# Optimization experiments

Measured on AMD Instinct MI355X. Metric: run time of the kernel, lower is better.

## Reference

```python
import jax, jax.numpy as jnp
import numpy as np

VOC, MEM, NSLOTS, NSENT, MAXLEN, QLEN, ANSLEN, B = 32000, 128, 20, 128, 32, 16, 8, 64


def _xavier(k, shape):
    fan_out, fan_in = shape
    std = jnp.sqrt(2.0 / (fan_in + fan_out))
    return (jax.random.normal(k, shape, jnp.float32) * std).astype(jnp.float32)


def setup_inputs() -> dict:
    key = jax.random.key(0)
    ks = jax.random.split(key, 12)
    inp = {}
    inp["input_ids"] = jax.random.randint(ks[0], (B, NSENT, MAXLEN), 0, VOC)
    inp["question"] = jax.random.randint(ks[1], (B, QLEN), 0, VOC)
    inp["ans"] = jax.random.randint(ks[2], (B, ANSLEN, 2), 0, VOC)
    E = jax.random.normal(ks[3], (VOC, MEM), jnp.float32)
    inp["E"] = E.at[0].set(0.0)  # padding_idx=0
    inp["Uw"] = _xavier(ks[4], (MEM, MEM)); inp["Ub"] = jnp.zeros((MEM,), jnp.float32)
    inp["Vw"] = _xavier(ks[5], (MEM, MEM)); inp["Vb"] = jnp.zeros((MEM,), jnp.float32)
    inp["Ww"] = _xavier(ks[6], (MEM, MEM)); inp["Wb"] = jnp.zeros((MEM,), jnp.float32)
    inp["slot_keys"] = jax.random.normal(ks[7], (NSLOTS, MEM), jnp.float32)  # self.w
    inp["Hw"] = _xavier(ks[8], (MEM, MEM)); inp["Hb"] = jnp.zeros((MEM,), jnp.float32)
    return inp


def reference(input_ids, question, ans, E, Uw, Ub, Vw, Vb, Ww, Wb, slot_keys, Hw, Hb):
    E0 = E.at[0].set(0.0)  # padding row stays zero
    bsz = input_ids.shape[0]
    n_sent = input_ids.shape[1]
    tok = input_ids.reshape(bsz, -1)
    # original indexes s[:, t, :] for t < n_sent over the flattened story
    s = E0[tok[:, :n_sent]]                       # [B, T, m]
    Ws = jnp.einsum('btm,nm->btn', s, Ww) + Wb    # precompute W(s_t): [B, T, m]
    Vkey = slot_keys @ Vw.T + Vb                  # [J, m]

    def step(mem, xs):
        # mem: [B, J, m]
        s_t, ws_t = xs                            # [B, m], [B, m]
        g = jax.nn.sigmoid(jnp.einsum('bm,bjm->bj', s_t, mem) + s_t @ slot_keys.T)  # [B, J]
        h_cand = jax.nn.relu(
            jnp.einsum('bjm,nm->bjn', mem, Uw) + Ub
            + Vkey[None, :, :] + ws_t[:, None, :]
        )  # dropout is identity in eval mode
        mem = mem + g[..., None] * h_cand
        # torch.norm(mem_j): global Frobenius norm over (batch, mem) per slot
        norms = jnp.sqrt(jnp.sum(mem * mem, axis=(0, 2), keepdims=True))
        return mem / norms, None

    mem0 = jnp.zeros((bsz, slot_keys.shape[0], s.shape[-1]), s.dtype)
    h, _ = jax.lax.scan(step, mem0, (jnp.swapaxes(s, 0, 1), jnp.swapaxes(Ws, 0, 1)))
    # output module
    q = E0[question].mean(1)                      # [B, m]
    a1 = E0[ans[:, :, 0]].mean(1)                 # [B, m]
    a2 = E0[ans[:, :, 1]].mean(1)                 # [B, m]
    p = jax.nn.softmax(jnp.einsum('bjm,bm->bj', h, q), axis=-1)   # [B, J]
    u = jnp.einsum('bj,bjm->bm', p, h)            # [B, m]
    r = jax.nn.relu(q + u @ Hw.T + Hb)            # [B, m]
    y1 = jnp.sum(r * a1, axis=1)
    y2 = jnp.sum(r * a2, axis=1)
    return jax.nn.softmax(jnp.stack((y1, y2), axis=1), axis=1)
```

## Files before the change

### kernel.cpp

```cpp
#include <hip/hip_runtime.h>
#include <math.h>


typedef __attribute__((ext_vector_type(8)))  short bf16x8;
typedef __attribute__((ext_vector_type(16))) float f32x16;
typedef __attribute__((ext_vector_type(2)))  float f32x2;

__device__ __forceinline__ unsigned short f2bh(float x) {
    unsigned int u = __float_as_uint(x);
    u += 0x7FFFu + ((u >> 16) & 1u);
    return (unsigned short)(u >> 16);
}
__device__ __forceinline__ unsigned int packtr(float lo, float hi) {
    return (__float_as_uint(lo) >> 16) | (__float_as_uint(hi) & 0xFFFF0000u);
}
__device__ __forceinline__ float blo(unsigned int w) { return __uint_as_float(w << 16); }
__device__ __forceinline__ float bhi(unsigned int w) { return __uint_as_float(w & 0xFFFF0000u); }

__device__ __forceinline__ f32x2 pkfma(f32x2 a, f32x2 b, f32x2 c) {
    return __builtin_elementwise_fma(a, b, c);
}
__device__ __forceinline__ f32x2 pkmax0(f32x2 a) {
    return __builtin_elementwise_max(a, (f32x2){0.f, 0.f});
}

#if __has_builtin(__builtin_amdgcn_fdot2_f32_bf16)
typedef __attribute__((ext_vector_type(2))) __bf16 bf16x2v;
__device__ __forceinline__ float dot2bf(unsigned int a, unsigned int b, float c) {
    return __builtin_amdgcn_fdot2_f32_bf16(
        __builtin_bit_cast(bf16x2v, a), __builtin_bit_cast(bf16x2v, b), c, false);
}
#else
__device__ __forceinline__ float dot2bf(unsigned int a, unsigned int b, float c) {
    return fmaf(bhi(a), bhi(b), fmaf(blo(a), blo(b), c));
}
#endif

template<int CTRL>
__device__ __forceinline__ float dpp_add0(float x) {
    int y = __builtin_amdgcn_update_dpp(0, __float_as_int(x), CTRL, 0xF, 0xF, true);
    return x + __int_as_float(y);
}
__device__ __forceinline__ float dpp_xor1_move(float x) {
    int y = __builtin_amdgcn_update_dpp(0, __float_as_int(x), 0xB1, 0xF, 0xF, true);
    return __int_as_float(y);
}

#define LDS_BARRIER() do {                                   \
    asm volatile("s_waitcnt lgkmcnt(0)" ::: "memory");       \
    __builtin_amdgcn_s_barrier();                            \
    asm volatile("" ::: "memory");                           \
} while (0)

__global__ __launch_bounds__(128) void prep_kernel(
    const int* __restrict__ ids, const int* __restrict__ ques, const int* __restrict__ ans,
    const float* __restrict__ E, const float* __restrict__ Ww, const float* __restrict__ Wb,
    const float* __restrict__ Vw, const float* __restrict__ Vb, const float* __restrict__ skeys,
    unsigned short* __restrict__ sT2, float* __restrict__ WsT, float* __restrict__ vkey,
    float* __restrict__ qv, float* __restrict__ a1v, float* __restrict__ a2v,
    float* __restrict__ SK)
{
    const int bi  = blockIdx.x;
    const int tid = threadIdx.x;
    __shared__ float s_l[8][132];
    __shared__ float sk_l[20 * 132];
    __shared__ float k_l[128];
    if (bi < 1024) {
        const int b = bi >> 4;
        const int g = bi & 15;
        for (int r = tid; r < 2560; r += 128) sk_l[(r >> 7) * 132 + (r & 127)] = skeys[r];
        for (int tt = 0; tt < 8; ++tt) {
            const int t     = g * 8 + tt;
            const int token = ids[b * 4096 + t];
            const float v   = E[token * 128 + tid];
            s_l[tt][tid] = v;
            sT2[(t * 64 + b) * 128 + tid] = f2bh(v);
        }
        __syncthreads();
        float acc[8];
        const float wbn = Wb[tid];
        #pragma unroll
        for (int i = 0; i < 8; ++i) acc[i] = wbn;
        const float4* wrow = (const float4*)(Ww + tid * 128);
        for (int m4 = 0; m4 < 32; ++m4) {
            const float4 w = wrow[m4];
            #pragma unroll
            for (int tt = 0; tt < 8; ++tt) {
                acc[tt] += s_l[tt][m4*4+0]*w.x + s_l[tt][m4*4+1]*w.y
                         + s_l[tt][m4*4+2]*w.z + s_l[tt][m4*4+3]*w.w;
            }
        }
        for (int tt = 0; tt < 8; ++tt)
            WsT[((g*8+tt) * 64 + b) * 128 + tid] = acc[tt];
        for (int idx = tid; idx < 160; idx += 128) {
            const int tt = idx / 20;
            const int jj = idx - tt * 20;
            float d = 0.f;
            for (int m = 0; m < 128; ++m) d += s_l[tt][m] * sk_l[jj * 132 + m];
            SK[(jj * 128 + (g*8 + tt)) * 64 + b] = d;
        }
    } else if (bi < 1044) {
        const int j = bi - 1024;
        k_l[tid] = skeys[j * 128 + tid];
        __syncthreads();
        float acc = Vb[tid];
        const float4* vrow = (const float4*)(Vw + tid * 128);
        for (int m4 = 0; m4 < 32; ++m4) {
            const float4 w = vrow[m4];
            acc += k_l[m4*4]*w.x + k_l[m4*4+1]*w.y + k_l[m4*4+2]*w.z + k_l[m4*4+3]*w.w;
        }
        vkey[j * 128 + tid] = acc;
    } else {
        const int b = bi - 1044;
        float sq = 0.f, s1 = 0.f, s2 = 0.f;
        for (int i = 0; i < 16; ++i) sq += E[ques[b*16+i] * 128 + tid];
        for (int i = 0; i < 8;  ++i) s1 += E[ans[(b*8+i)*2+0] * 128 + tid];
        for (int i = 0; i < 8;  ++i) s2 += E[ans[(b*8+i)*2+1] * 128 + tid];
        qv [b*128+tid] = sq * (1.f/16.f);
        a1v[b*128+tid] = s1 * 0.125f;
        a2v[b*128+tid] = s2 * 0.125f;
    }
}

__global__ __launch_bounds__(512, 1) void scan_kernel(
    const unsigned short* __restrict__ sT2, const float* __restrict__ WsT,
    const float* __restrict__ vkey, const float* __restrict__ Uw,
    const float* __restrict__ Ub, const float* __restrict__ SK,
    float* __restrict__ h_out)
{
    __shared__ unsigned short AB[64 * 136];
    __shared__ float g_l[64];
    __shared__ float wred[8];

    const int j    = blockIdx.x;
    const int tid  = threadIdx.x;
    const int wave = tid >> 6;
    const int lane = tid & 63;
    const int l32  = lane & 31;
    const int q    = lane >> 5;
    const int bt2  = wave & 1;
    const int nt2  = wave >> 1;
    const int n    = nt2 * 32 + l32;
    const int gb   = tid >> 3;
    const int gm   = (tid & 7) * 16;
    const bool evenl = ((l32 & 1) == 0);

    bf16x8 b_h[8];
    {
        const int k0 = q * 8;
        #pragma unroll
        for (int kc = 0; kc < 8; ++kc) {
            const float4* src = (const float4*)(Uw + n * 128 + kc * 16 + k0);
            const float4 v0 = src[0], v1 = src[1];
            const float xs[8] = {v0.x,v0.y,v0.z,v0.w, v1.x,v1.y,v1.z,v1.w};
            #pragma unroll
            for (int e = 0; e < 8; ++e) b_h[kc][e] = (short)f2bh(xs[e]);
        }
    }
    for (int i = tid; i < 64 * 136 / 2; i += 512) ((unsigned int*)AB)[i] = 0u;
    const float ubv = Ub[n] + vkey[j * 128 + n];

    unsigned woffB[16];
    #pragma unroll
    for (int r = 0; r < 16; ++r) {
        const int brow = bt2*32 + 4*q + (r & 3) + 8*(r >> 2);
        woffB[r] = (unsigned)((brow * 128 + n) * 4);
    }
    const unsigned soffB = (unsigned)((gb * 128 + gm) * 2);
    const unsigned koffB = (unsigned)(gb * 4);
    const char* SKj = (const char*)SK + (size_t)j * 32768;
    unsigned* const wdst = (unsigned*)((char*)AB
        + (bt2*32 + 4*q + ((l32 & 1) << 4)) * 272 + ((n & ~1) * 2));

    f32x2 xprev2[8];
    #pragma unroll
    for (int p = 0; p < 8; ++p) xprev2[p] = (f32x2){0.f, 0.f};
#define XV(k) ((k) & 1 ? xprev2[(k) >> 1].y : xprev2[(k) >> 1].x)

    uint4 svA0, svA1, svB0, svB1;
    float skvA, skvB;
    float wsv[16];
    {
        const char* pS = (const char*)sT2 + soffB;
        svA0 = *(const uint4*)(pS); svA1 = *(const uint4*)(pS + 16);
        skvA = *(const float*)(SKj + koffB);
        const char* pW = (const char*)WsT;
        #pragma unroll
        for (int r = 0; r < 16; ++r) wsv[r] = *(const float*)(pW + woffB[r]);
    }
    __syncthreads();

    float inv_s = 1.f;

#define SCAN_STEP(T_CUR, Sc0,Sc1,SKc, Sn0,Sn1,SKn)                             \
    {                                                                          \
        const int tn = (T_CUR < 127) ? (T_CUR) + 1 : 127;                      \
                        \
        {                                                                      \
            const char* pS = (const char*)sT2 + (size_t)tn * 16384 + soffB;    \
            Sn0 = *(const uint4*)(pS); Sn1 = *(const uint4*)(pS + 16);         \
            SKn = *(const float*)(SKj + (size_t)tn * 256 + koffB);             \
        }                                                                      \
               \
        {                                                                      \
            const uint4* u4 = (const uint4*)(AB + gb * 136 + gm);              \
            const uint4 w0 = u4[0], w1 = u4[1];                                \
            float d0 = dot2bf(w0.x, Sc0.x, 0.f);                               \
            float d1 = dot2bf(w0.y, Sc0.y, 0.f);                               \
            float d2 = dot2bf(w0.z, Sc0.z, 0.f);                               \
            float d3 = dot2bf(w0.w, Sc0.w, 0.f);                               \
            d0 = dot2bf(w1.x, Sc1.x, d0);                                      \
            d1 = dot2bf(w1.y, Sc1.y, d1);                                      \
            d2 = dot2bf(w1.z, Sc1.z, d2);                                      \
            d3 = dot2bf(w1.w, Sc1.w, d3);                                      \
            float dg = (d0 + d1) + (d2 + d3);                                  \
            dg = dpp_add0<0x111>(dg);                           \
            dg = dpp_add0<0x112>(dg);                           \
            dg = dpp_add0<0x114>(dg);          \
            if ((tid & 7) == 7) {                                              \
                const float e = __expf(-(inv_s * dg + SKc));                   \
                g_l[gb] = __builtin_amdgcn_rcpf(1.f + e);                      \
            }                                                                  \
        }                                                                      \
                         \
        f32x16 acc0 = {0.f,0.f,0.f,0.f,0.f,0.f,0.f,0.f,                        \
                       0.f,0.f,0.f,0.f,0.f,0.f,0.f,0.f};                       \
        f32x16 acc1 = acc0;                                                    \
        {                                                                      \
            const unsigned short* arow = AB + (bt2*32 + l32) * 136 + q * 8;    \
            _Pragma("unroll")                                                  \
            for (int kc = 0; kc < 8; ++kc) {                                   \
                const bf16x8 a = *(const bf16x8*)(arow + kc * 16);             \
                if (kc & 1) acc1 = __builtin_amdgcn_mfma_f32_32x32x16_bf16(a, b_h[kc], acc1, 0, 0, 0); \
                else        acc0 = __builtin_amdgcn_mfma_f32_32x32x16_bf16(a, b_h[kc], acc0, 0, 0, 0); \
            }                                                                  \
            acc0 += acc1;    \
        }                                                                      \
        LDS_BARRIER();                 \
                 \
        const float4 gA = *(const float4*)(g_l + bt2*32 + 4*q + 0);            \
        const float4 gB = *(const float4*)(g_l + bt2*32 + 4*q + 8);            \
        const float4 gC = *(const float4*)(g_l + bt2*32 + 4*q + 16);           \
        const float4 gD = *(const float4*)(g_l + bt2*32 + 4*q + 24);           \
        const f32x2 g2[8] = {{gA.x,gA.y},{gA.z,gA.w},{gB.x,gB.y},{gB.z,gB.w},  \
                             {gC.x,gC.y},{gC.z,gC.w},{gD.x,gD.y},{gD.z,gD.w}}; \
        const f32x2 inv2 = {inv_s, inv_s};                                     \
        const f32x2 ub2  = {ubv, ubv};                                         \
        f32x2 ssqv = {0.f, 0.f};                                               \
        _Pragma("unroll")                                                      \
        for (int p = 0; p < 8; ++p) {                                          \
            const f32x2 am = {acc0[2*p], acc0[2*p+1]};                         \
            const f32x2 wu = (f32x2){wsv[2*p], wsv[2*p+1]} + ub2;              \
            f32x2 hr = pkfma(inv2, am, wu);                                    \
            hr = pkmax0(hr);                                       \
            const f32x2 x = pkfma(inv2, xprev2[p], hr * g2[p]);                \
            xprev2[p] = x;                                \
            ssqv = pkfma(x, x, ssqv);                                          \
        }                                                                      \
               \
        _Pragma("unroll")                                                      \
        for (int i = 0; i < 8; ++i) {                                          \
            const float xa = XV(i);                                            \
            const float xb = XV(i + 8);                                        \
            const float sa = dpp_xor1_move(xa);                                \
            const float sb = dpp_xor1_move(xb);                                \
            const float lo = evenl ? xa : sb;                                  \
            const float hi = evenl ? sa : xb;                                  \
            wdst[((i & 3) + 8 * (i >> 2)) * 68] = packtr(lo, hi);              \
        }                                                                      \
            \
        {                                                                      \
            const char* pW = (const char*)WsT + (size_t)tn * 32768;            \
            _Pragma("unroll")                                                  \
            for (int r = 0; r < 16; ++r)                                       \
                wsv[r] = *(const float*)(pW + woffB[r]);                       \
        }                                                                      \
                 \
        float ssq = ssqv.x + ssqv.y;                                           \
        ssq = dpp_add0<0x111>(ssq);                             \
        ssq = dpp_add0<0x112>(ssq);                             \
        ssq = dpp_add0<0x114>(ssq);                             \
        ssq = dpp_add0<0x118>(ssq);       \
        ssq = dpp_add0<0x142>(ssq);     \
        ssq = dpp_add0<0x143>(ssq);          \
        if (lane == 63) wred[wave] = ssq;                                      \
        LDS_BARRIER();     \
        const float4 w0 = *(const float4*)(wred);                              \
        const float4 w1 = *(const float4*)(wred + 4);                          \
        const float4 ws4 = w0 + w1;                                            \
        inv_s = __builtin_amdgcn_rsqf((ws4.x + ws4.y) + (ws4.z + ws4.w));      \
    }

    for (int t = 0; t < 128; t += 2) {
        SCAN_STEP(t,     svA0,svA1,skvA, svB0,svB1,skvB)
        SCAN_STEP(t + 1, svB0,svB1,skvB, svA0,svA1,skvA)
    }
#undef SCAN_STEP

    #pragma unroll
    for (int r = 0; r < 16; ++r) {
        const int brow = bt2*32 + 4*q + (r & 3) + 8*(r >> 2);
        h_out[(brow*20 + j)*128 + n] = inv_s * XV(r);
    }
#undef XV
}

__global__ __launch_bounds__(128) void final_kernel(
    const float* __restrict__ h, const float* __restrict__ qv,
    const float* __restrict__ a1v, const float* __restrict__ a2v,
    const float* __restrict__ Hw, const float* __restrict__ Hb,
    float* __restrict__ out)
{
    const int b   = blockIdx.x;
    const int tid = threadIdx.x;
    __shared__ float hb[20][128];
    __shared__ float ql[128];
    __shared__ float ul[128];
    __shared__ float pl[20];
    __shared__ float lgt[20];
    __shared__ float red1[2], red2[2];

    for (int jj = 0; jj < 20; ++jj) hb[jj][tid] = h[(b*20+jj)*128 + tid];
    ql[tid] = qv[b*128 + tid];
    __syncthreads();
    if (tid < 20) {
        float d = 0.f;
        for (int m = 0; m < 128; ++m) d += hb[tid][m] * ql[m];
        lgt[tid] = d;
    }
    __syncthreads();
    if (tid == 0) {
        float mx = lgt[0];
        for (int jj = 1; jj < 20; ++jj) mx = fmaxf(mx, lgt[jj]);
        float s = 0.f;
        for (int jj = 0; jj < 20; ++jj) { const float e = expf(lgt[jj]-mx); pl[jj] = e; s += e; }
        const float is = 1.f / s;
        for (int jj = 0; jj < 20; ++jj) pl[jj] *= is;
    }
    __syncthreads();
    float u = 0.f;
    for (int jj = 0; jj < 20; ++jj) u += pl[jj] * hb[jj][tid];
    ul[tid] = u;
    __syncthreads();
    float acc = ql[tid] + Hb[tid];
    const float4* hwr = (const float4*)(Hw + tid*128);
    for (int m4 = 0; m4 < 32; ++m4) {
        const float4 w = hwr[m4];
        acc += ul[m4*4]*w.x + ul[m4*4+1]*w.y + ul[m4*4+2]*w.z + ul[m4*4+3]*w.w;
    }
    const float r  = fmaxf(acc, 0.f);
    float y1 = r * a1v[b*128+tid];
    float y2 = r * a2v[b*128+tid];
    #pragma unroll
    for (int mask = 1; mask < 64; mask <<= 1) {
        y1 += __shfl_xor(y1, mask, 64);
        y2 += __shfl_xor(y2, mask, 64);
    }
    if ((tid & 63) == 0) { red1[tid>>6] = y1; red2[tid>>6] = y2; }
    __syncthreads();
    if (tid == 0) {
        const float z1 = red1[0] + red1[1];
        const float z2 = red2[0] + red2[1];
        const float mx = fmaxf(z1, z2);
        const float e1 = expf(z1-mx), e2 = expf(z2-mx);
        const float s  = e1 + e2;
        out[b*2+0] = e1 / s;
        out[b*2+1] = e2 / s;
    }
}

extern "C" void kernel_launch(void* const* d_in, const int* in_sizes, int n_in,
                              void* d_out, int out_size, void* d_ws, size_t ws_size,
                              hipStream_t stream)
{
    const int*   ids  = (const int*)  d_in[0];
    const int*   ques = (const int*)  d_in[1];
    const int*   ans  = (const int*)  d_in[2];
    const float* E    = (const float*)d_in[3];
    const float* Uw   = (const float*)d_in[4];
    const float* Ubv  = (const float*)d_in[5];
    const float* Vw   = (const float*)d_in[6];
    const float* Vb   = (const float*)d_in[7];
    const float* Ww   = (const float*)d_in[8];
    const float* Wb   = (const float*)d_in[9];
    const float* sk   = (const float*)d_in[10];
    const float* Hw   = (const float*)d_in[11];
    const float* Hb   = (const float*)d_in[12];

    float* ws   = (float*)d_ws;
    unsigned short* sT2 = (unsigned short*)ws;
    float* WsT  = ws    + 524288;
    float* vkey = WsT   + 1048576;
    float* qv   = vkey  + 2560;
    float* a1v  = qv    + 8192;
    float* a2v  = a1v   + 8192;
    float* h    = a2v   + 8192;
    float* SK   = h     + 163840;

    prep_kernel<<<1108, 128, 0, stream>>>(ids, ques, ans, E, Ww, Wb, Vw, Vb, sk,
                                          sT2, WsT, vkey, qv, a1v, a2v, SK);
    scan_kernel<<<20, 512, 0, stream>>>(sT2, WsT, vkey, Uw, Ubv, SK, h);
    final_kernel<<<64, 128, 0, stream>>>(h, qv, a1v, a2v, Hw, Hb, (float*)d_out);
}
```

Before: 261.2 us.

## Halve scan block to 256 threads, each wave computing two N-tiles

The sequential scan kernel now uses 4 waves instead of 8. Each wave computes two 32-column output tiles with two MFMA chains, and the gate dot product is split across 4 lanes instead of 8. The goal is cheaper per-step barriers and cross-wave reductions on the 128-step serial chain, and more independent MFMA work per wave. The cost is twice the per-wave MFMA and elementwise work on the critical path, plus higher register pressure.

```diff
diff --git a/kernel.cpp b/kernel.cpp
--- a/kernel.cpp
+++ b/kernel.cpp
@@ -122,7 +122,7 @@
     }
 }
 
-__global__ __launch_bounds__(512, 1) void scan_kernel(
+__global__ __launch_bounds__(256, 1) void scan_kernel(
     const unsigned short* __restrict__ sT2, const float* __restrict__ WsT,
     const float* __restrict__ vkey, const float* __restrict__ Uw,
     const float* __restrict__ Ub, const float* __restrict__ SK,
@@ -130,7 +130,7 @@
 {
     __shared__ unsigned short AB[64 * 136];
     __shared__ float g_l[64];
-    __shared__ float wred[8];
+    __shared__ float wred[4];
 
     const int j    = blockIdx.x;
     const int tid  = threadIdx.x;
@@ -139,102 +139,131 @@
     const int l32  = lane & 31;
     const int q    = lane >> 5;
     const int bt2  = wave & 1;
-    const int nt2  = wave >> 1;
-    const int n    = nt2 * 32 + l32;
-    const int gb   = tid >> 3;
-    const int gm   = (tid & 7) * 16;
+    const int nt1  = wave >> 1;
+    const int nA   = nt1 * 64 + l32;
+    const int gb   = tid >> 2;
+    const int gm32 = (tid & 3) * 32;
     const bool evenl = ((l32 & 1) == 0);
 
-    bf16x8 b_h[8];
+    bf16x8 b_hA[8], b_hB[8];
     {
         const int k0 = q * 8;
         #pragma unroll
         for (int kc = 0; kc < 8; ++kc) {
-            const float4* src = (const float4*)(Uw + n * 128 + kc * 16 + k0);
-            const float4 v0 = src[0], v1 = src[1];
-            const float xs[8] = {v0.x,v0.y,v0.z,v0.w, v1.x,v1.y,v1.z,v1.w};
-            #pragma unroll
-            for (int e = 0; e < 8; ++e) b_h[kc][e] = (short)f2bh(xs[e]);
-        }
-    }
-    for (int i = tid; i < 64 * 136 / 2; i += 512) ((unsigned int*)AB)[i] = 0u;
-    const float ubv = Ub[n] + vkey[j * 128 + n];
+            {
+                const float4* src = (const float4*)(Uw + nA * 128 + kc * 16 + k0);
+                const float4 v0 = src[0], v1 = src[1];
+                const float xs[8] = {v0.x,v0.y,v0.z,v0.w, v1.x,v1.y,v1.z,v1.w};
+                #pragma unroll
+                for (int e = 0; e < 8; ++e) b_hA[kc][e] = (short)f2bh(xs[e]);
+            }
+            {
+                const float4* src = (const float4*)(Uw + (nA + 32) * 128 + kc * 16 + k0);
+                const float4 v0 = src[0], v1 = src[1];
+                const float xs[8] = {v0.x,v0.y,v0.z,v0.w, v1.x,v1.y,v1.z,v1.w};
+                #pragma unroll
+                for (int e = 0; e < 8; ++e) b_hB[kc][e] = (short)f2bh(xs[e]);
+            }
+        }
+    }
+    for (int i = tid; i < 64 * 136 / 2; i += 256) ((unsigned int*)AB)[i] = 0u;
+    const float ubvA = Ub[nA]      + vkey[j * 128 + nA];
+    const float ubvB = Ub[nA + 32] + vkey[j * 128 + nA + 32];
 
     unsigned woffB[16];
     #pragma unroll
     for (int r = 0; r < 16; ++r) {
         const int brow = bt2*32 + 4*q + (r & 3) + 8*(r >> 2);
-        woffB[r] = (unsigned)((brow * 128 + n) * 4);
-    }
-    const unsigned soffB = (unsigned)((gb * 128 + gm) * 2);
+        woffB[r] = (unsigned)((brow * 128 + nA) * 4);
+    }
+    const unsigned soffB = (unsigned)(gb * 256 + gm32 * 2);
     const unsigned koffB = (unsigned)(gb * 4);
     const char* SKj = (const char*)SK + (size_t)j * 32768;
-    unsigned* const wdst = (unsigned*)((char*)AB
-        + (bt2*32 + 4*q + ((l32 & 1) << 4)) * 272 + ((n & ~1) * 2));
-
-    f32x2 xprev2[8];
+    unsigned* const wdstA = (unsigned*)((char*)AB
+        + (bt2*32 + 4*q + ((l32 & 1) << 4)) * 272 + ((nA & ~1) * 2));
+
+    f32x2 xprevA[8], xprevB[8];
     #pragma unroll
-    for (int p = 0; p < 8; ++p) xprev2[p] = (f32x2){0.f, 0.f};
-#define XV(k) ((k) & 1 ? xprev2[(k) >> 1].y : xprev2[(k) >> 1].x)
-
-    uint4 svA0, svA1, svB0, svB1;
-    float skvA, skvB;
-    float wsv[16];
+    for (int p = 0; p < 8; ++p) { xprevA[p] = (f32x2){0.f,0.f}; xprevB[p] = (f32x2){0.f,0.f}; }
+#define XVA(k) ((k) & 1 ? xprevA[(k) >> 1].y : xprevA[(k) >> 1].x)
+#define XVB(k) ((k) & 1 ? xprevB[(k) >> 1].y : xprevB[(k) >> 1].x)
+
+    uint4 svP[4], svQ[4];
+    float skvP, skvQ;
+    float wsvA[16], wsvB[16];
     {
         const char* pS = (const char*)sT2 + soffB;
-        svA0 = *(const uint4*)(pS); svA1 = *(const uint4*)(pS + 16);
-        skvA = *(const float*)(SKj + koffB);
+        #pragma unroll
+        for (int i = 0; i < 4; ++i) svP[i] = *(const uint4*)(pS + i * 16);
+        skvP = *(const float*)(SKj + koffB);
         const char* pW = (const char*)WsT;
         #pragma unroll
-        for (int r = 0; r < 16; ++r) wsv[r] = *(const float*)(pW + woffB[r]);
+        for (int r = 0; r < 16; ++r) {
+            wsvA[r] = *(const float*)(pW + woffB[r]);
+            wsvB[r] = *(const float*)(pW + woffB[r] + 128);
+        }
     }
     __syncthreads();
 
     float inv_s = 1.f;
 
-#define SCAN_STEP(T_CUR, Sc0,Sc1,SKc, Sn0,Sn1,SKn)                             \
+#define SCAN_STEP(T_CUR, SCc, SKc, SCn, SKn)                                   \
     {                                                                          \
         const int tn = (T_CUR < 127) ? (T_CUR) + 1 : 127;                      \
                         \
         {                                                                      \
             const char* pS = (const char*)sT2 + (size_t)tn * 16384 + soffB;    \
-            Sn0 = *(const uint4*)(pS); Sn1 = *(const uint4*)(pS + 16);         \
+            _Pragma("unroll")                                                  \
+            for (int i = 0; i < 4; ++i) SCn[i] = *(const uint4*)(pS + i * 16); \
             SKn = *(const float*)(SKj + (size_t)tn * 256 + koffB);             \
         }                                                                      \
                \
         {                                                                      \
-            const uint4* u4 = (const uint4*)(AB + gb * 136 + gm);              \
-            const uint4 w0 = u4[0], w1 = u4[1];                                \
-            float d0 = dot2bf(w0.x, Sc0.x, 0.f);                               \
-            float d1 = dot2bf(w0.y, Sc0.y, 0.f);                               \
-            float d2 = dot2bf(w0.z, Sc0.z, 0.f);                               \
-            float d3 = dot2bf(w0.w, Sc0.w, 0.f);                               \
-            d0 = dot2bf(w1.x, Sc1.x, d0);                                      \
-            d1 = dot2bf(w1.y, Sc1.y, d1);                                      \
-            d2 = dot2bf(w1.z, Sc1.z, d2);                                      \
-            d3 = dot2bf(w1.w, Sc1.w, d3);                                      \
+            const uint4* u4 = (const uint4*)(AB + gb * 136 + gm32);            \
+            const uint4 u0 = u4[0], u1 = u4[1], u2 = u4[2], u3 = u4[3];        \
+            float d0 = dot2bf(u0.x, SCc[0].x, 0.f);                            \
+            float d1 = dot2bf(u0.y, SCc[0].y, 0.f);                            \
+            float d2 = dot2bf(u0.z, SCc[0].z, 0.f);                            \
+            float d3 = dot2bf(u0.w, SCc[0].w, 0.f);                            \
+            d0 = dot2bf(u1.x, SCc[1].x, d0);                                   \
+            d1 = dot2bf(u1.y, SCc[1].y, d1);                                   \
+            d2 = dot2bf(u1.z, SCc[1].z, d2);                                   \
+            d3 = dot2bf(u1.w, SCc[1].w, d3);                                   \
+            d0 = dot2bf(u2.x, SCc[2].x, d0);                                   \
+            d1 = dot2bf(u2.y, SCc[2].y, d1);                                   \
+            d2 = dot2bf(u2.z, SCc[2].z, d2);                                   \
+            d3 = dot2bf(u2.w, SCc[2].w, d3);                                   \
+            d0 = dot2bf(u3.x, SCc[3].x, d0);                                   \
+            d1 = dot2bf(u3.y, SCc[3].y, d1);                                   \
+            d2 = dot2bf(u3.z, SCc[3].z, d2);                                   \
+            d3 = dot2bf(u3.w, SCc[3].w, d3);                                   \
             float dg = (d0 + d1) + (d2 + d3);                                  \
             dg = dpp_add0<0x111>(dg);                           \
-            dg = dpp_add0<0x112>(dg);                           \
-            dg = dpp_add0<0x114>(dg);          \
-            if ((tid & 7) == 7) {                                              \
+            dg = dpp_add0<0x112>(dg);          \
+            if ((tid & 3) == 3) {                                              \
                 const float e = __expf(-(inv_s * dg + SKc));                   \
                 g_l[gb] = __builtin_amdgcn_rcpf(1.f + e);                      \
             }                                                                  \
         }                                                                      \
-                         \
-        f32x16 acc0 = {0.f,0.f,0.f,0.f,0.f,0.f,0.f,0.f,                        \
-                       0.f,0.f,0.f,0.f,0.f,0.f,0.f,0.f};                       \
-        f32x16 acc1 = acc0;                                                    \
+                                   \
+        f32x16 accA0 = {0.f,0.f,0.f,0.f,0.f,0.f,0.f,0.f,                       \
+                        0.f,0.f,0.f,0.f,0.f,0.f,0.f,0.f};                      \
+        f32x16 accA1 = accA0, accB0 = accA0, accB1 = accA0;                    \
         {                                                                      \
             const unsigned short* arow = AB + (bt2*32 + l32) * 136 + q * 8;    \
             _Pragma("unroll")                                                  \
             for (int kc = 0; kc < 8; ++kc) {                                   \
                 const bf16x8 a = *(const bf16x8*)(arow + kc * 16);             \
-                if (kc & 1) acc1 = __builtin_amdgcn_mfma_f32_32x32x16_bf16(a, b_h[kc], acc1, 0, 0, 0); \
-                else        acc0 = __builtin_amdgcn_mfma_f32_32x32x16_bf16(a, b_h[kc], acc0, 0, 0, 0); \
+                if (kc & 1) {                                                  \
+                    accA1 = __builtin_amdgcn_mfma_f32_32x32x16_bf16(a, b_hA[kc], accA1, 0, 0, 0); \
+                    accB1 = __builtin_amdgcn_mfma_f32_32x32x16_bf16(a, b_hB[kc], accB1, 0, 0, 0); \
+                } else {                                                       \
+                    accA0 = __builtin_amdgcn_mfma_f32_32x32x16_bf16(a, b_hA[kc], accA0, 0, 0, 0); \
+                    accB0 = __builtin_amdgcn_mfma_f32_32x32x16_bf16(a, b_hB[kc], accB0, 0, 0, 0); \
+                }                                                              \
             }                                                                  \
-            acc0 += acc1;    \
+            accA0 += accA1;                                                    \
+            accB0 += accB1;                                                    \
         }                                                                      \
         LDS_BARRIER();                 \
                  \
@@ -245,35 +274,55 @@
         const f32x2 g2[8] = {{gA.x,gA.y},{gA.z,gA.w},{gB.x,gB.y},{gB.z,gB.w},  \
                              {gC.x,gC.y},{gC.z,gC.w},{gD.x,gD.y},{gD.z,gD.w}}; \
         const f32x2 inv2 = {inv_s, inv_s};                                     \
-        const f32x2 ub2  = {ubv, ubv};                                         \
+        const f32x2 ubA2 = {ubvA, ubvA};                                       \
+        const f32x2 ubB2 = {ubvB, ubvB};                                       \
         f32x2 ssqv = {0.f, 0.f};                                               \
         _Pragma("unroll")                                                      \
         for (int p = 0; p < 8; ++p) {                                          \
-            const f32x2 am = {acc0[2*p], acc0[2*p+1]};                         \
-            const f32x2 wu = (f32x2){wsv[2*p], wsv[2*p+1]} + ub2;              \
-            f32x2 hr = pkfma(inv2, am, wu);                                    \
-            hr = pkmax0(hr);                                       \
-            const f32x2 x = pkfma(inv2, xprev2[p], hr * g2[p]);                \
-            xprev2[p] = x;                                \
-            ssqv = pkfma(x, x, ssqv);                                          \
-        }                                                                      \
-               \
+            const f32x2 amA = {accA0[2*p], accA0[2*p+1]};                      \
+            const f32x2 wuA = (f32x2){wsvA[2*p], wsvA[2*p+1]} + ubA2;          \
+            f32x2 hrA = pkfma(inv2, amA, wuA);                                 \
+            hrA = pkmax0(hrA);                                                 \
+            const f32x2 xA = pkfma(inv2, xprevA[p], hrA * g2[p]);              \
+            xprevA[p] = xA;                                                    \
+            ssqv = pkfma(xA, xA, ssqv);                                        \
+            const f32x2 amB = {accB0[2*p], accB0[2*p+1]};                      \
+            const f32x2 wuB = (f32x2){wsvB[2*p], wsvB[2*p+1]} + ubB2;          \
+            f32x2 hrB = pkfma(inv2, amB, wuB);                                 \
+            hrB = pkmax0(hrB);                                                 \
+            const f32x2 xB = pkfma(inv2, xprevB[p], hrB * g2[p]);              \
+            xprevB[p] = xB;                                                    \
+            ssqv = pkfma(xB, xB, ssqv);                                        \
+        }                                                                      \
+           \
         _Pragma("unroll")                                                      \
         for (int i = 0; i < 8; ++i) {                                          \
-            const float xa = XV(i);                                            \
-            const float xb = XV(i + 8);                                        \
-            const float sa = dpp_xor1_move(xa);                                \
-            const float sb = dpp_xor1_move(xb);                                \
-            const float lo = evenl ? xa : sb;                                  \
-            const float hi = evenl ? sa : xb;                                  \
-            wdst[((i & 3) + 8 * (i >> 2)) * 68] = packtr(lo, hi);              \
+            const int wo = ((i & 3) + 8 * (i >> 2)) * 68;                      \
+            {                                                                  \
+                const float xa = XVA(i), xb = XVA(i + 8);                      \
+                const float sa = dpp_xor1_move(xa);                            \
+                const float sb = dpp_xor1_move(xb);                            \
+                const float lo = evenl ? xa : sb;                              \
+                const float hi = evenl ? sa : xb;                              \
+                wdstA[wo] = packtr(lo, hi);                                    \
+            }                                                                  \
+            {                                                                  \
+                const float xa = XVB(i), xb = XVB(i + 8);                      \
+                const float sa = dpp_xor1_move(xa);                            \
+                const float sb = dpp_xor1_move(xb);                            \
+                const float lo = evenl ? xa : sb;                              \
+                const float hi = evenl ? sa : xb;                              \
+                wdstA[wo + 16] = packtr(lo, hi);            \
+            }                                                                  \
         }                                                                      \
             \
         {                                                                      \
             const char* pW = (const char*)WsT + (size_t)tn * 32768;            \
             _Pragma("unroll")                                                  \
-            for (int r = 0; r < 16; ++r)                                       \
-                wsv[r] = *(const float*)(pW + woffB[r]);                       \
+            for (int r = 0; r < 16; ++r) {                                     \
+                wsvA[r] = *(const float*)(pW + woffB[r]);                      \
+                wsvB[r] = *(const float*)(pW + woffB[r] + 128);                \
+            }                                                                  \
         }                                                                      \
                  \
         float ssq = ssqv.x + ssqv.y;                                           \
@@ -286,23 +335,23 @@
         if (lane == 63) wred[wave] = ssq;                                      \
         LDS_BARRIER();     \
         const float4 w0 = *(const float4*)(wred);                              \
-        const float4 w1 = *(const float4*)(wred + 4);                          \
-        const float4 ws4 = w0 + w1;                                            \
-        inv_s = __builtin_amdgcn_rsqf((ws4.x + ws4.y) + (ws4.z + ws4.w));      \
+        inv_s = __builtin_amdgcn_rsqf((w0.x + w0.y) + (w0.z + w0.w));          \
     }
 
     for (int t = 0; t < 128; t += 2) {
-        SCAN_STEP(t,     svA0,svA1,skvA, svB0,svB1,skvB)
-        SCAN_STEP(t + 1, svB0,svB1,skvB, svA0,svA1,skvA)
+        SCAN_STEP(t,     svP, skvP, svQ, skvQ)
+        SCAN_STEP(t + 1, svQ, skvQ, svP, skvP)
     }
 #undef SCAN_STEP
 
     #pragma unroll
     for (int r = 0; r < 16; ++r) {
         const int brow = bt2*32 + 4*q + (r & 3) + 8*(r >> 2);
-        h_out[(brow*20 + j)*128 + n] = inv_s * XV(r);
-    }
-#undef XV
+        h_out[(brow*20 + j)*128 + nA]      = inv_s * XVA(r);
+        h_out[(brow*20 + j)*128 + nA + 32] = inv_s * XVB(r);
+    }
+#undef XVA
+#undef XVB
 }
 
 __global__ __launch_bounds__(128) void final_kernel(
@@ -399,6 +448,6 @@
 
     prep_kernel<<<1108, 128, 0, stream>>>(ids, ques, ans, E, Ww, Wb, Vw, Vb, sk,
                                           sT2, WsT, vkey, qv, a1v, a2v, SK);
-    scan_kernel<<<20, 512, 0, stream>>>(sT2, WsT, vkey, Uw, Ubv, SK, h);
+    scan_kernel<<<20, 256, 0, stream>>>(sT2, WsT, vkey, Uw, Ubv, SK, h);
     final_kernel<<<64, 128, 0, stream>>>(h, qv, a1v, a2v, Hw, Hb, (float*)d_out);
 }
```

Result: slower. 313.5 us (+20.0%).

## Double-buffer memory tile and use 16x16 MFMA to drop a per-step barrier

Applied to the files above, without the earlier changes.

Rewrites the recurrent scan step to use 16x16x32 bf16 MFMAs with a new wave/tile mapping, so each wave's gate values depend only on rows it computes itself. The gate reduction now uses shuffles and a per-wave LDS slot instead of a block-wide g_l array. The memory tile is ping-ponged between two LDS buffers, which removes one of the two block barriers per timestep. Each wave now keeps more B-fragments in registers, and the launch bound is raised to allow two blocks per CU. The risks are register pressure and correctness of the new fragment layout.

```diff
diff --git a/kernel.cpp b/kernel.cpp
--- a/kernel.cpp
+++ b/kernel.cpp
@@ -3,7 +3,7 @@
 
 
 typedef __attribute__((ext_vector_type(8)))  short bf16x8;
-typedef __attribute__((ext_vector_type(16))) float f32x16;
+typedef __attribute__((ext_vector_type(4)))  float f32x4;
 typedef __attribute__((ext_vector_type(2)))  float f32x2;
 
 __device__ __forceinline__ unsigned short f2bh(float x) {
@@ -122,186 +122,210 @@
     }
 }
 
-__global__ __launch_bounds__(512, 1) void scan_kernel(
+__global__ __launch_bounds__(512, 2) void scan_kernel(
     const unsigned short* __restrict__ sT2, const float* __restrict__ WsT,
     const float* __restrict__ vkey, const float* __restrict__ Uw,
     const float* __restrict__ Ub, const float* __restrict__ SK,
     float* __restrict__ h_out)
 {
-    __shared__ unsigned short AB[64 * 136];
-    __shared__ float g_l[64];
-    __shared__ float wred[8];
+    __shared__ unsigned short AB0[64 * 136];
+    __shared__ unsigned short AB1[64 * 136];
+    __shared__ float g_w[8][16];
+    __shared__ float wredA[8], wredB[8];
 
     const int j    = blockIdx.x;
     const int tid  = threadIdx.x;
     const int wave = tid >> 6;
     const int lane = tid & 63;
-    const int l32  = lane & 31;
-    const int q    = lane >> 5;
-    const int bt2  = wave & 1;
-    const int nt2  = wave >> 1;
-    const int n    = nt2 * 32 + l32;
-    const int gb   = tid >> 3;
-    const int gm   = (tid & 7) * 16;
-    const bool evenl = ((l32 & 1) == 0);
-
-    bf16x8 b_h[8];
-    {
-        const int k0 = q * 8;
-        #pragma unroll
-        for (int kc = 0; kc < 8; ++kc) {
-            const float4* src = (const float4*)(Uw + n * 128 + kc * 16 + k0);
+    const int c16  = lane & 15;
+    const int kg   = lane >> 4;
+    const int rg   = wave >> 1;
+    const int cg   = wave & 1;
+    const int brow_a = rg * 16 + c16;
+    const bool evenl = ((c16 & 1) == 0);
+
+    bf16x8 b_h[4][4];
+    #pragma unroll
+    for (int tl = 0; tl < 4; ++tl) {
+        const int n = cg * 64 + tl * 16 + c16;
+        #pragma unroll
+        for (int kc = 0; kc < 4; ++kc) {
+            const float4* src = (const float4*)(Uw + n * 128 + kc * 32 + kg * 8);
             const float4 v0 = src[0], v1 = src[1];
             const float xs[8] = {v0.x,v0.y,v0.z,v0.w, v1.x,v1.y,v1.z,v1.w};
             #pragma unroll
-            for (int e = 0; e < 8; ++e) b_h[kc][e] = (short)f2bh(xs[e]);
-        }
-    }
-    for (int i = tid; i < 64 * 136 / 2; i += 512) ((unsigned int*)AB)[i] = 0u;
-    const float ubv = Ub[n] + vkey[j * 128 + n];
-
-    unsigned woffB[16];
-    #pragma unroll
-    for (int r = 0; r < 16; ++r) {
-        const int brow = bt2*32 + 4*q + (r & 3) + 8*(r >> 2);
-        woffB[r] = (unsigned)((brow * 128 + n) * 4);
-    }
-    const unsigned soffB = (unsigned)((gb * 128 + gm) * 2);
-    const unsigned koffB = (unsigned)(gb * 4);
+            for (int e = 0; e < 8; ++e) b_h[tl][kc][e] = (short)f2bh(xs[e]);
+        }
+    }
+    for (int i = tid; i < 64 * 136 / 2; i += 512) {
+        ((unsigned int*)AB0)[i] = 0u;
+        ((unsigned int*)AB1)[i] = 0u;
+    }
+
+    float ubv[4];
+    #pragma unroll
+    for (int tl = 0; tl < 4; ++tl) {
+        const int n = cg * 64 + tl * 16 + c16;
+        ubv[tl] = Ub[n] + vkey[j * 128 + n];
+    }
+    unsigned woff[16];
+    #pragma unroll
+    for (int tl = 0; tl < 4; ++tl)
+        #pragma unroll
+        for (int reg = 0; reg < 4; ++reg) {
+            const int b = rg * 16 + kg * 4 + reg;
+            const int n = cg * 64 + tl * 16 + c16;
+            woff[tl * 4 + reg] = (unsigned)((b * 128 + n) * 4);
+        }
+    const unsigned sfoff = (unsigned)(brow_a * 256 + kg * 16);
+    const unsigned skoff = (unsigned)(brow_a * 4);
     const char* SKj = (const char*)SK + (size_t)j * 32768;
-    unsigned* const wdst = (unsigned*)((char*)AB
-        + (bt2*32 + 4*q + ((l32 & 1) << 4)) * 272 + ((n & ~1) * 2));
+    const int wbidx = (rg*16 + kg*4 + (evenl ? 0 : 2)) * 68 + cg*32 + (c16 >> 1);
+    unsigned* const wb0 = (unsigned*)AB0 + wbidx;
+    unsigned* const wb1 = (unsigned*)AB1 + wbidx;
 
     f32x2 xprev2[8];
     #pragma unroll
     for (int p = 0; p < 8; ++p) xprev2[p] = (f32x2){0.f, 0.f};
-#define XV(k) ((k) & 1 ? xprev2[(k) >> 1].y : xprev2[(k) >> 1].x)
-
-    uint4 svA0, svA1, svB0, svB1;
+#define XV(reg, tl) ((reg) & 1 ? xprev2[(tl)*2 + ((reg)>>1)].y : xprev2[(tl)*2 + ((reg)>>1)].x)
+
+    uint4 sfA[4], sfB[4];
     float skvA, skvB;
     float wsv[16];
     {
-        const char* pS = (const char*)sT2 + soffB;
-        svA0 = *(const uint4*)(pS); svA1 = *(const uint4*)(pS + 16);
-        skvA = *(const float*)(SKj + koffB);
+        const char* pS = (const char*)sT2 + sfoff;
+        #pragma unroll
+        for (int kc = 0; kc < 4; ++kc) sfA[kc] = *(const uint4*)(pS + kc * 64);
+        skvA = *(const float*)(SKj + skoff);
         const char* pW = (const char*)WsT;
         #pragma unroll
-        for (int r = 0; r < 16; ++r) wsv[r] = *(const float*)(pW + woffB[r]);
+        for (int r = 0; r < 16; ++r) wsv[r] = *(const float*)(pW + woff[r]);
     }
     __syncthreads();
 
     float inv_s = 1.f;
 
-#define SCAN_STEP(T_CUR, Sc0,Sc1,SKc, Sn0,Sn1,SKn)                             \
+#define SCAN_STEP(T_CUR, ABc, WB, WRED, SFc, SKVc, SFn, SKVn)                  \
     {                                                                          \
         const int tn = (T_CUR < 127) ? (T_CUR) + 1 : 127;                      \
                         \
         {                                                                      \
-            const char* pS = (const char*)sT2 + (size_t)tn * 16384 + soffB;    \
-            Sn0 = *(const uint4*)(pS); Sn1 = *(const uint4*)(pS + 16);         \
-            SKn = *(const float*)(SKj + (size_t)tn * 256 + koffB);             \
-        }                                                                      \
-               \
+            const char* pS = (const char*)sT2 + (size_t)tn * 16384 + sfoff;    \
+            _Pragma("unroll")                                                  \
+            for (int kc = 0; kc < 4; ++kc) SFn[kc] = *(const uint4*)(pS + kc * 64); \
+            SKVn = *(const float*)(SKj + (size_t)tn * 256 + skoff);            \
+        }                                                                      \
+          \
+        uint4 w[4];                                                            \
         {                                                                      \
-            const uint4* u4 = (const uint4*)(AB + gb * 136 + gm);              \
-            const uint4 w0 = u4[0], w1 = u4[1];                                \
-            float d0 = dot2bf(w0.x, Sc0.x, 0.f);                               \
-            float d1 = dot2bf(w0.y, Sc0.y, 0.f);                               \
-            float d2 = dot2bf(w0.z, Sc0.z, 0.f);                               \
-            float d3 = dot2bf(w0.w, Sc0.w, 0.f);                               \
-            d0 = dot2bf(w1.x, Sc1.x, d0);                                      \
-            d1 = dot2bf(w1.y, Sc1.y, d1);                                      \
-            d2 = dot2bf(w1.z, Sc1.z, d2);                                      \
-            d3 = dot2bf(w1.w, Sc1.w, d3);                                      \
-            float dg = (d0 + d1) + (d2 + d3);                                  \
-            dg = dpp_add0<0x111>(dg);                           \
-            dg = dpp_add0<0x112>(dg);                           \
-            dg = dpp_add0<0x114>(dg);          \
-            if ((tid & 7) == 7) {                                              \
-                const float e = __expf(-(inv_s * dg + SKc));                   \
-                g_l[gb] = __builtin_amdgcn_rcpf(1.f + e);                      \
+            const unsigned short* ar = ABc + brow_a * 136 + kg * 8;            \
+            _Pragma("unroll")                                                  \
+            for (int kc = 0; kc < 4; ++kc) w[kc] = *(const uint4*)(ar + kc * 32); \
+        }                                                                      \
+           \
+        f32x4 acc[4];                                                          \
+        _Pragma("unroll")                                                      \
+        for (int tl = 0; tl < 4; ++tl) acc[tl] = (f32x4){0.f,0.f,0.f,0.f};     \
+        _Pragma("unroll")                                                      \
+        for (int kc = 0; kc < 4; ++kc) {                                       \
+            const bf16x8 a = __builtin_bit_cast(bf16x8, w[kc]);                \
+            _Pragma("unroll")                                                  \
+            for (int tl = 0; tl < 4; ++tl)                                     \
+                acc[tl] = __builtin_amdgcn_mfma_f32_16x16x32_bf16(a, b_h[tl][kc], acc[tl], 0, 0, 0); \
+        }                                                                      \
+            \
+        {                                                                      \
+            float d0 = dot2bf(w[0].x, SFc[0].x, 0.f);                          \
+            float d1 = dot2bf(w[0].y, SFc[0].y, 0.f);                          \
+            float d2 = dot2bf(w[0].z, SFc[0].z, 0.f);                          \
+            float d3 = dot2bf(w[0].w, SFc[0].w, 0.f);                          \
+            _Pragma("unroll")                                                  \
+            for (int kc = 1; kc < 4; ++kc) {                                   \
+                d0 = dot2bf(w[kc].x, SFc[kc].x, d0);                           \
+                d1 = dot2bf(w[kc].y, SFc[kc].y, d1);                           \
+                d2 = dot2bf(w[kc].z, SFc[kc].z, d2);                           \
+                d3 = dot2bf(w[kc].w, SFc[kc].w, d3);                           \
             }                                                                  \
-        }                                                                      \
-                         \
-        f32x16 acc0 = {0.f,0.f,0.f,0.f,0.f,0.f,0.f,0.f,                        \
-                       0.f,0.f,0.f,0.f,0.f,0.f,0.f,0.f};                       \
-        f32x16 acc1 = acc0;                                                    \
-        {                                                                      \
-            const unsigned short* arow = AB + (bt2*32 + l32) * 136 + q * 8;    \
-            _Pragma("unroll")                                                  \
-            for (int kc = 0; kc < 8; ++kc) {                                   \
-                const bf16x8 a = *(const bf16x8*)(arow + kc * 16);             \
-                if (kc & 1) acc1 = __builtin_amdgcn_mfma_f32_32x32x16_bf16(a, b_h[kc], acc1, 0, 0, 0); \
-                else        acc0 = __builtin_amdgcn_mfma_f32_32x32x16_bf16(a, b_h[kc], acc0, 0, 0, 0); \
+            float dd = (d0 + d1) + (d2 + d3);                                  \
+            dd += __shfl_xor(dd, 16, 64);                                      \
+            dd += __shfl_xor(dd, 32, 64);                                      \
+            if (kg == 0) {                                                     \
+                const float e = __expf(-(inv_s * dd + SKVc));                  \
+                g_w[wave][c16] = __builtin_amdgcn_rcpf(1.f + e);               \
             }                                                                  \
-            acc0 += acc1;    \
-        }                                                                      \
-        LDS_BARRIER();                 \
-                 \
-        const float4 gA = *(const float4*)(g_l + bt2*32 + 4*q + 0);            \
-        const float4 gB = *(const float4*)(g_l + bt2*32 + 4*q + 8);            \
-        const float4 gC = *(const float4*)(g_l + bt2*32 + 4*q + 16);           \
-        const float4 gD = *(const float4*)(g_l + bt2*32 + 4*q + 24);           \
-        const f32x2 g2[8] = {{gA.x,gA.y},{gA.z,gA.w},{gB.x,gB.y},{gB.z,gB.w},  \
-                             {gC.x,gC.y},{gC.z,gC.w},{gD.x,gD.y},{gD.z,gD.w}}; \
+        }                                                                      \
+        asm volatile("s_waitcnt lgkmcnt(0)" ::: "memory");    \
+        const float4 g4 = *(const float4*)(&g_w[wave][kg * 4]);                \
+            \
         const f32x2 inv2 = {inv_s, inv_s};                                     \
-        const f32x2 ub2  = {ubv, ubv};                                         \
         f32x2 ssqv = {0.f, 0.f};                                               \
         _Pragma("unroll")                                                      \
-        for (int p = 0; p < 8; ++p) {                                          \
-            const f32x2 am = {acc0[2*p], acc0[2*p+1]};                         \
-            const f32x2 wu = (f32x2){wsv[2*p], wsv[2*p+1]} + ub2;              \
-            f32x2 hr = pkfma(inv2, am, wu);                                    \
-            hr = pkmax0(hr);                                       \
-            const f32x2 x = pkfma(inv2, xprev2[p], hr * g2[p]);                \
-            xprev2[p] = x;                                \
-            ssqv = pkfma(x, x, ssqv);                                          \
-        }                                                                      \
-               \
+        for (int tl = 0; tl < 4; ++tl) {                                       \
+            const f32x2 ub2 = {ubv[tl], ubv[tl]};                              \
+            _Pragma("unroll")                                                  \
+            for (int rp = 0; rp < 2; ++rp) {                                   \
+                const int p = tl * 2 + rp;                                     \
+                const f32x2 am = {acc[tl][2*rp], acc[tl][2*rp+1]};             \
+                const f32x2 wu = (f32x2){wsv[tl*4+2*rp], wsv[tl*4+2*rp+1]} + ub2; \
+                f32x2 hr = pkfma(inv2, am, wu);                                \
+                hr = pkmax0(hr);                                               \
+                const f32x2 gg = rp ? (f32x2){g4.z, g4.w} : (f32x2){g4.x, g4.y}; \
+                const f32x2 x = pkfma(inv2, xprev2[p], hr * gg);               \
+                xprev2[p] = x;                                                 \
+                ssqv = pkfma(x, x, ssqv);                                      \
+            }                                                                  \
+        }                                                                      \
+           \
         _Pragma("unroll")                                                      \
-        for (int i = 0; i < 8; ++i) {                                          \
-            const float xa = XV(i);                                            \
-            const float xb = XV(i + 8);                                        \
-            const float sa = dpp_xor1_move(xa);                                \
-            const float sb = dpp_xor1_move(xb);                                \
-            const float lo = evenl ? xa : sb;                                  \
-            const float hi = evenl ? sa : xb;                                  \
-            wdst[((i & 3) + 8 * (i >> 2)) * 68] = packtr(lo, hi);              \
+        for (int tl = 0; tl < 4; ++tl) {                                       \
+            const float s0 = dpp_xor1_move(XV(0, tl));                         \
+            const float s1 = dpp_xor1_move(XV(1, tl));                         \
+            const float s2 = dpp_xor1_move(XV(2, tl));                         \
+            const float s3 = dpp_xor1_move(XV(3, tl));                         \
+            const float loA = evenl ? XV(0, tl) : s2;                          \
+            const float hiA = evenl ? s0        : XV(2, tl);                   \
+            const float loB = evenl ? XV(1, tl) : s3;                          \
+            const float hiB = evenl ? s1        : XV(3, tl);                   \
+            WB[tl * 8]      = packtr(loA, hiA);                                \
+            WB[68 + tl * 8] = packtr(loB, hiB);                                \
         }                                                                      \
             \
         {                                                                      \
             const char* pW = (const char*)WsT + (size_t)tn * 32768;            \
             _Pragma("unroll")                                                  \
             for (int r = 0; r < 16; ++r)                                       \
-                wsv[r] = *(const float*)(pW + woffB[r]);                       \
+                wsv[r] = *(const float*)(pW + woff[r]);                        \
         }                                                                      \
                  \
         float ssq = ssqv.x + ssqv.y;                                           \
-        ssq = dpp_add0<0x111>(ssq);                             \
-        ssq = dpp_add0<0x112>(ssq);                             \
-        ssq = dpp_add0<0x114>(ssq);                             \
-        ssq = dpp_add0<0x118>(ssq);       \
-        ssq = dpp_add0<0x142>(ssq);     \
-        ssq = dpp_add0<0x143>(ssq);          \
-        if (lane == 63) wred[wave] = ssq;                                      \
-        LDS_BARRIER();     \
-        const float4 w0 = *(const float4*)(wred);                              \
-        const float4 w1 = *(const float4*)(wred + 4);                          \
-        const float4 ws4 = w0 + w1;                                            \
-        inv_s = __builtin_amdgcn_rsqf((ws4.x + ws4.y) + (ws4.z + ws4.w));      \
+        ssq = dpp_add0<0x111>(ssq);                                            \
+        ssq = dpp_add0<0x112>(ssq);                                            \
+        ssq = dpp_add0<0x114>(ssq);                                            \
+        ssq = dpp_add0<0x118>(ssq);                                            \
+        ssq = dpp_add0<0x142>(ssq);                                            \
+        ssq = dpp_add0<0x143>(ssq);                                            \
+        if (lane == 63) WRED[wave] = ssq;                                      \
+        LDS_BARRIER();               \
+        const float4 q0 = *(const float4*)(WRED);                              \
+        const float4 q1 = *(const float4*)(WRED + 4);                          \
+        const float4 qs = q0 + q1;                                             \
+        inv_s = __builtin_amdgcn_rsqf((qs.x + qs.y) + (qs.z + qs.w));          \
     }
 
     for (int t = 0; t < 128; t += 2) {
-        SCAN_STEP(t,     svA0,svA1,skvA, svB0,svB1,skvB)
-        SCAN_STEP(t + 1, svB0,svB1,skvB, svA0,svA1,skvA)
+        SCAN_STEP(t,     AB0, wb1, wredA, sfA, skvA, sfB, skvB)
+        SCAN_STEP(t + 1, AB1, wb0, wredB, sfB, skvB, sfA, skvA)
     }
 #undef SCAN_STEP
 
     #pragma unroll
-    for (int r = 0; r < 16; ++r) {
-        const int brow = bt2*32 + 4*q + (r & 3) + 8*(r >> 2);
-        h_out[(brow*20 + j)*128 + n] = inv_s * XV(r);
-    }
+    for (int tl = 0; tl < 4; ++tl)
+        #pragma unroll
+        for (int reg = 0; reg < 4; ++reg) {
+            const int b = rg * 16 + kg * 4 + reg;
+            const int n = cg * 64 + tl * 16 + c16;
+            h_out[((size_t)b * 20 + j) * 128 + n] = inv_s * XV(reg, tl);
+        }
 #undef XV
 }
 
```

New measurement: 282.2 us. 8.0% more time.
